# Kernel optimization log

Measured on AMD Instinct MI355X. Metric: run time of the kernel, lower is better.

Reference implementation:

```python
import jax, jax.numpy as jnp
import numpy as np

N = 50000
E = 800000
B = 64
NODE_IN, EDGE_IN, H, OUT_DIM = 16, 8, 64, 2


def _glorot(key, shape):
    fan_in, fan_out = shape[0], shape[-1]
    s = jnp.sqrt(6.0 / (fan_in + fan_out))
    return jax.random.uniform(key, shape, jnp.float32, -s, s)


def setup_inputs() -> dict:
    key = jax.random.key(0)
    ks = jax.random.split(key, 32)
    inp = {
        'x': jax.random.normal(ks[0], (N, NODE_IN), jnp.float32),
        'edge_index': jax.random.randint(ks[1], (2, E), 0, N).astype(jnp.int64),
        'edge_attr': jax.random.normal(ks[2], (E, EDGE_IN), jnp.float32),
        'batch': jnp.sort(jax.random.randint(ks[3], (N,), 0, B)).astype(jnp.int64),
        # encoders
        'W_node': _glorot(ks[4], (NODE_IN, H)), 'b_node': jnp.zeros((H,), jnp.float32),
        'W_edge': _glorot(ks[5], (EDGE_IN, H)), 'b_edge': jnp.zeros((H,), jnp.float32),
        # conv1: GATv2, heads=4, concat=True, edge_dim=H
        'Wl1': _glorot(ks[6], (H, 4 * H)), 'bl1': jnp.zeros((4 * H,), jnp.float32),
        'Wr1': _glorot(ks[7], (H, 4 * H)), 'br1': jnp.zeros((4 * H,), jnp.float32),
        'We1': _glorot(ks[8], (H, 4 * H)),
        'att1': _glorot(ks[9], (4, H)),
        'bias1': jnp.zeros((4 * H,), jnp.float32),
        # conv2: GATv2, heads=1, concat=False, in=4H
        'Wl2': _glorot(ks[10], (4 * H, H)), 'bl2': jnp.zeros((H,), jnp.float32),
        'Wr2': _glorot(ks[11], (4 * H, H)), 'br2': jnp.zeros((H,), jnp.float32),
        'We2': _glorot(ks[12], (H, H)),
        'att2': _glorot(ks[13], (1, H)),
        'bias2': jnp.zeros((H,), jnp.float32),
        # decoder
        'Wd1': _glorot(ks[14], (H, H)), 'bd1': jnp.zeros((H,), jnp.float32),
        'Wd2': _glorot(ks[15], (H, OUT_DIM)), 'bd2': jnp.zeros((OUT_DIM,), jnp.float32),
    }
    return inp


def _gatv2(x, src, dst, eattr, Wl, bl, Wr, br, We, att, bias, heads, out_ch, concat):
    n = x.shape[0]
    # add self-loops with edge_attr fill_value='mean' (segment mean over dst), PyG default
    ones = jnp.ones((src.shape[0],), x.dtype)
    deg = jax.ops.segment_sum(ones, dst, num_segments=n)
    loop_attr = jax.ops.segment_sum(eattr, dst, num_segments=n) / jnp.clip(deg, 1.0)[:, None]
    ea = jnp.concatenate([eattr, loop_attr], 0)               # [E+N, F_e]
    s = jnp.concatenate([src, jnp.arange(n)], 0)
    d = jnp.concatenate([dst, jnp.arange(n)], 0)
    xl = (x @ Wl + bl).reshape(n, heads, out_ch)              # source transform
    xr = (x @ Wr + br).reshape(n, heads, out_ch)              # target transform
    ep = (ea @ We).reshape(-1, heads, out_ch)                 # edge transform (no bias)
    m = jax.nn.leaky_relu(xl[s] + xr[d] + ep, 0.2)            # [E+N, heads, out_ch]
    logits = jnp.einsum('ehc,hc->eh', m, att)
    lmax = jax.ops.segment_max(logits, d, num_segments=n)
    lmax = jnp.where(jnp.isfinite(lmax), lmax, 0.0)
    a = jnp.exp(logits - lmax[d])
    denom = jax.ops.segment_sum(a, d, num_segments=n)
    alpha = a / (denom[d] + 1e-16)                            # segment softmax over dst
    out = jax.ops.segment_sum(alpha[..., None] * xl[s], d, num_segments=n)
    out = out.reshape(n, heads * out_ch) if concat else out.mean(1)
    return out + bias


def reference(x, edge_index, edge_attr, batch, W_node, b_node, W_edge, b_edge,
              Wl1, bl1, Wr1, br1, We1, att1, bias1,
              Wl2, bl2, Wr2, br2, We2, att2, bias2,
              Wd1, bd1, Wd2, bd2):
    src, dst = edge_index[0], edge_index[1]
    h = x @ W_node + b_node
    ea = edge_attr @ W_edge + b_edge
    h = jax.nn.elu(_gatv2(h, src, dst, ea, Wl1, bl1, Wr1, br1, We1, att1, bias1, 4, H, True))
    h = _gatv2(h, src, dst, ea, Wl2, bl2, Wr2, br2, We2, att2, bias2, 1, H, False)
    # global mean pool over batch vector
    cnt = jax.ops.segment_sum(jnp.ones((h.shape[0],), h.dtype), batch, num_segments=B)
    pooled = jax.ops.segment_sum(h, batch, num_segments=B) / jnp.clip(cnt, 1.0)[:, None]
    out = jax.nn.relu(pooled @ Wd1 + bd1) @ Wd2 + bd2
    return jax.nn.sigmoid(out)
```

## Files before the change

### kernel.cpp

```cpp
#include <hip/hip_runtime.h>
#include <math.h>

#define NN 50000
#define NE 800000
#define NB 64

__device__ __forceinline__ int permpos(int c) {
  return ((c & 63) << 2) | (((c >> 6) ^ c) & 3);
}

__device__ __forceinline__ unsigned short f2bf(float f) {
  unsigned int u = __float_as_uint(f);
  u += 0x7fffu + ((u >> 16) & 1u);
  return (unsigned short)(u >> 16);
}
__device__ __forceinline__ float bf2f(unsigned short b) {
  return __uint_as_float(((unsigned int)b) << 16);
}

__global__ void k_zero(int* __restrict__ p, int n) {
  int i = blockIdx.x * blockDim.x + threadIdx.x;
  if (i < n) p[i] = 0;
}

__global__ void k_fuse(const float* __restrict__ Wn, const float* __restrict__ bn,
                       const float* __restrict__ We, const float* __restrict__ be,
                       const float* __restrict__ Wl1, const float* __restrict__ bl1,
                       const float* __restrict__ Wr1, const float* __restrict__ br1,
                       const float* __restrict__ We1, const float* __restrict__ We2,
                       const float* __restrict__ att1, const float* __restrict__ bias1,
                       float* __restrict__ wl1e, float* __restrict__ bl1e,
                       float* __restrict__ wr1e, float* __restrict__ br1e,
                       float* __restrict__ wfe1, float* __restrict__ bfe1,
                       float* __restrict__ wfe2, float* __restrict__ bfe2,
                       float* __restrict__ att1p, float* __restrict__ bias1p) {
  int t = blockIdx.x * blockDim.x + threadIdx.x;
  if (t < 4096) {
    int i = t >> 8, j = t & 255; float s = 0.f;
    for (int k = 0; k < 64; k++) s += Wn[i * 64 + k] * Wl1[k * 256 + j];
    wl1e[i * 256 + permpos(j)] = s;
  } else if (t < 8192) {
    int u = t - 4096; int i = u >> 8, j = u & 255; float s = 0.f;
    for (int k = 0; k < 64; k++) s += Wn[i * 64 + k] * Wr1[k * 256 + j];
    wr1e[i * 256 + permpos(j)] = s;
  } else if (t < 10240) {
    int u = t - 8192; int i = u >> 8, j = u & 255; float s = 0.f;
    for (int k = 0; k < 64; k++) s += We[i * 64 + k] * We1[k * 256 + j];
    wfe1[i * 256 + permpos(j)] = s;
  } else if (t < 10752) {
    int u = t - 10240; int i = u >> 6, j = u & 63; float s = 0.f;
    for (int k = 0; k < 64; k++) s += We[i * 64 + k] * We2[k * 64 + j];
    wfe2[u] = s;
  } else if (t < 11008) {
    int j = t - 10752; float s = bl1[j];
    for (int k = 0; k < 64; k++) s += bn[k] * Wl1[k * 256 + j];
    bl1e[permpos(j)] = s;
  } else if (t < 11264) {
    int j = t - 11008; float s = br1[j];
    for (int k = 0; k < 64; k++) s += bn[k] * Wr1[k * 256 + j];
    br1e[permpos(j)] = s;
  } else if (t < 11520) {
    int j = t - 11264; float s = 0.f;
    for (int k = 0; k < 64; k++) s += be[k] * We1[k * 256 + j];
    bfe1[permpos(j)] = s;
  } else if (t < 11584) {
    int j = t - 11520; float s = 0.f;
    for (int k = 0; k < 64; k++) s += be[k] * We2[k * 64 + j];
    bfe2[j] = s;
  } else if (t < 11840) {
    int j = t - 11584;
    att1p[permpos(j)] = att1[j];
  } else if (t < 12096) {
    int j = t - 11840;
    bias1p[permpos(j)] = bias1[j];
  }
}

__global__ void k_deg(const int* __restrict__ dstA, int* __restrict__ deg) {
  int e = blockIdx.x * blockDim.x + threadIdx.x;
  if (e < NE) atomicAdd(&deg[dstA[e]], 1);
}

__global__ __launch_bounds__(1024) void k_scan1(const int* __restrict__ deg,
                                                int* __restrict__ incl, int* __restrict__ partials) {
  __shared__ int sm[1024];
  int i = blockIdx.x * 1024 + threadIdx.x;
  int v = (i < NN) ? (deg[i] + 1) : 0;
  sm[threadIdx.x] = v;
  __syncthreads();
  for (int off = 1; off < 1024; off <<= 1) {
    int t = (threadIdx.x >= off) ? sm[threadIdx.x - off] : 0;
    __syncthreads();
    sm[threadIdx.x] += t;
    __syncthreads();
  }
  if (i < NN) incl[i] = sm[threadIdx.x];
  if (threadIdx.x == 1023) partials[blockIdx.x] = sm[1023];
}

__global__ void k_scan2(int* __restrict__ partials, int* __restrict__ rowptr, int nblk) {
  int t = threadIdx.x;
  int v = (t < nblk) ? partials[t] : 0;
  for (int off = 1; off < 64; off <<= 1) {
    int u = __shfl_up(v, off, 64);
    if (t >= off) v += u;
  }
  if (t < nblk) partials[t] = v;
  if (t == nblk - 1) rowptr[NN] = v;
}

__global__ void k_scan3(const int* __restrict__ deg, const int* __restrict__ incl,
                        const int* __restrict__ partials, int* __restrict__ rowptr) {
  int i = blockIdx.x * blockDim.x + threadIdx.x;
  if (i >= NN) return;
  int blk = i >> 10;
  int base = blk ? partials[blk - 1] : 0;
  rowptr[i] = base + incl[i] - (deg[i] + 1);
}

__global__ void k_csr(const int* __restrict__ srcA, const int* __restrict__ dstA,
                      const int* __restrict__ rowptr, const int* __restrict__ deg,
                      int* __restrict__ cursor, int2* __restrict__ csr) {
  int t = blockIdx.x * blockDim.x + threadIdx.x;
  if (t < NE) {
    int d = dstA[t];
    int pos = rowptr[d] + atomicAdd(&cursor[d], 1);
    csr[pos] = make_int2(t, srcA[t]);
  } else if (t < NE + NN) {
    int n = t - NE;
    csr[rowptr[n] + deg[n]] = make_int2(NE + n, n);
  }
}

__global__ __launch_bounds__(256) void k_loop8(const int* __restrict__ rowptr,
                                               const int2* __restrict__ csr,
                                               const float* __restrict__ eattr,
                                               float* __restrict__ lattr) {
  int d = (blockIdx.x * blockDim.x + threadIdx.x) >> 6;
  int lane = threadIdx.x & 63;
  if (d >= NN) return;
  int beg = rowptr[d], endReal = rowptr[d + 1] - 1;
  int k = lane & 7, sub = lane >> 3;
  float s = 0.f;
  for (int i = beg + sub; i < endReal; i += 8) {
    int eid = csr[i].x;
    s += eattr[(size_t)eid * 8 + k];
  }
  s += __shfl_xor(s, 8, 64);
  s += __shfl_xor(s, 16, 64);
  s += __shfl_xor(s, 32, 64);
  float invdeg = 1.f / fmaxf((float)(endReal - beg), 1.f);
  if (lane < 8) lattr[(size_t)d * 8 + lane] = s * invdeg;
}

__global__ __launch_bounds__(256) void k_lin1(const float* __restrict__ x,
                                              const float* __restrict__ wl, const float* __restrict__ bl,
                                              const float* __restrict__ wr, const float* __restrict__ br,
                                              unsigned short* __restrict__ xl, float* __restrict__ xr) {
  __shared__ float xs[4][16];
  int nb = blockIdx.x * 4;
  int t = threadIdx.x;
  if (t < 64) xs[t >> 4][t & 15] = x[nb * 16 + t];
  __syncthreads();
  int w = t >> 6, lane = t & 63, l4 = lane << 2;
  float4 accl = *(const float4*)(bl + l4);
  float4 accr = *(const float4*)(br + l4);
  const float* xrow = xs[w];
#pragma unroll
  for (int k = 0; k < 16; k++) {
    float xv = xrow[k];
    float4 wl4 = *(const float4*)(wl + k * 256 + l4);
    float4 wr4 = *(const float4*)(wr + k * 256 + l4);
    accl.x += xv * wl4.x; accl.y += xv * wl4.y; accl.z += xv * wl4.z; accl.w += xv * wl4.w;
    accr.x += xv * wr4.x; accr.y += xv * wr4.y; accr.z += xv * wr4.z; accr.w += xv * wr4.w;
  }
  int node = nb + w;
  ushort4 us;
  us.x = f2bf(accl.x); us.y = f2bf(accl.y); us.z = f2bf(accl.z); us.w = f2bf(accl.w);
  *(ushort4*)(xl + (size_t)node * 256 + l4) = us;
  *(float4*)(xr + (size_t)node * 256 + l4) = accr;
}

__device__ __forceinline__ const float* ek_ptr(const float* __restrict__ eattr,
                                               const float* __restrict__ lattr, int eid) {
  return (eid < NE) ? (eattr + (size_t)eid * 8) : (lattr + (size_t)(eid - NE) * 8);
}

__device__ __forceinline__ float jreduce(float part[4]) {
  part[0] += __shfl_xor(part[1], 1, 64);
  part[2] += __shfl_xor(part[3], 1, 64);
  float v = part[0] + __shfl_xor(part[2], 2, 64);
  v += __shfl_xor(v, 4, 64);
  v += __shfl_xor(v, 8, 64);
  v += __shfl_xor(v, 16, 64);
  v += __shfl_xor(v, 32, 64);
  return v;
}

__global__ __launch_bounds__(256) void k_conv1(
    const float* __restrict__ eattr, const float* __restrict__ lattr,
    const int* __restrict__ rowptr, const int2* __restrict__ csr,
    const unsigned short* __restrict__ xl, const float* __restrict__ xrg,
    const float* __restrict__ att1p, const float* __restrict__ bias1p,
    const float* __restrict__ wfe1, const float* __restrict__ bfe1,
    float* __restrict__ out1) {
  int d = __builtin_amdgcn_readfirstlane((blockIdx.x * blockDim.x + threadIdx.x) >> 6);
  int lane = threadIdx.x & 63;
  if (d >= NN) return;
  int l4 = lane << 2;
  float4 xr4 = *(const float4*)(xrg + (size_t)d * 256 + l4);
  float4 at4 = *(const float4*)(att1p + l4);
  float4 bf4 = *(const float4*)(bfe1 + l4);
  float4 wf[8];
#pragma unroll
  for (int k = 0; k < 8; k++) wf[k] = *(const float4*)(wfe1 + k * 256 + l4);

  float acc0 = 0.f, acc1 = 0.f, acc2 = 0.f, acc3 = 0.f;
  float mrun = -INFINITY, lrun = 0.f;
  int beg = rowptr[d], end = rowptr[d + 1];

  auto ld4 = [&](int s) -> float4 {
    ushort4 u = *(const ushort4*)(xl + (size_t)s * 256 + l4);
    float4 f; f.x = bf2f(u.x); f.y = bf2f(u.y); f.z = bf2f(u.z); f.w = bf2f(u.w);
    return f;
  };
  auto epart = [&](const float* __restrict__ p, const float4& x4, float part[4]) {
    float e0 = bf4.x, e1 = bf4.y, e2 = bf4.z, e3 = bf4.w;
#pragma unroll
    for (int k = 0; k < 8; k++) {
      float ekv = p[k];
      e0 += ekv * wf[k].x; e1 += ekv * wf[k].y;
      e2 += ekv * wf[k].z; e3 += ekv * wf[k].w;
    }
    float m0 = x4.x + xr4.x + e0; m0 = (m0 > 0.f) ? m0 : 0.2f * m0;
    float m1 = x4.y + xr4.y + e1; m1 = (m1 > 0.f) ? m1 : 0.2f * m1;
    float m2 = x4.z + xr4.z + e2; m2 = (m2 > 0.f) ? m2 : 0.2f * m2;
    float m3 = x4.w + xr4.w + e3; m3 = (m3 > 0.f) ? m3 : 0.2f * m3;
    part[0] = at4.x * m0; part[1] = at4.y * m1;
    part[2] = at4.z * m2; part[3] = at4.w * m3;
  };

  int idx = beg;
  for (; idx + 4 <= end; idx += 4) {
    int2 e0 = csr[idx], e1 = csr[idx + 1], e2 = csr[idx + 2], e3 = csr[idx + 3];
    int s0 = __builtin_amdgcn_readfirstlane(e0.y), id0 = __builtin_amdgcn_readfirstlane(e0.x);
    int s1 = __builtin_amdgcn_readfirstlane(e1.y), id1 = __builtin_amdgcn_readfirstlane(e1.x);
    int s2 = __builtin_amdgcn_readfirstlane(e2.y), id2 = __builtin_amdgcn_readfirstlane(e2.x);
    int s3 = __builtin_amdgcn_readfirstlane(e3.y), id3 = __builtin_amdgcn_readfirstlane(e3.x);
    float4 x0 = ld4(s0), x1 = ld4(s1), x2 = ld4(s2), x3 = ld4(s3);
    float pa[4], pb[4], pc[4], pd[4];
    epart(ek_ptr(eattr, lattr, id0), x0, pa);
    epart(ek_ptr(eattr, lattr, id1), x1, pb);
    epart(ek_ptr(eattr, lattr, id2), x2, pc);
    epart(ek_ptr(eattr, lattr, id3), x3, pd);
    float v0 = jreduce(pa), v1 = jreduce(pb), v2 = jreduce(pc), v3 = jreduce(pd);
    float gmax = fmaxf(fmaxf(v0, v1), fmaxf(v2, v3));
    if (__ballot(gmax > mrun)) {
      float nm = fmaxf(mrun, gmax);
      float sc = __expf(mrun - nm);
      mrun = nm; lrun *= sc;
      float sc1 = __shfl_xor(sc, 1, 64);
      float sc2 = __shfl_xor(sc, 2, 64);
      float sc3 = __shfl_xor(sc1, 2, 64);
      acc0 *= sc; acc1 *= sc1; acc2 *= sc2; acc3 *= sc3;
    }
    float q0 = __expf(v0 - mrun), q1 = __expf(v1 - mrun);
    float q2 = __expf(v2 - mrun), q3 = __expf(v3 - mrun);
    lrun += q0 + q1 + q2 + q3;
    {
      float a1 = __shfl_xor(q0, 1, 64), a2 = __shfl_xor(q0, 2, 64), a3 = __shfl_xor(a1, 2, 64);
      acc0 += q0 * x0.x; acc1 += a1 * x0.y; acc2 += a2 * x0.z; acc3 += a3 * x0.w;
    }
    {
      float a1 = __shfl_xor(q1, 1, 64), a2 = __shfl_xor(q1, 2, 64), a3 = __shfl_xor(a1, 2, 64);
      acc0 += q1 * x1.x; acc1 += a1 * x1.y; acc2 += a2 * x1.z; acc3 += a3 * x1.w;
    }
    {
      float a1 = __shfl_xor(q2, 1, 64), a2 = __shfl_xor(q2, 2, 64), a3 = __shfl_xor(a1, 2, 64);
      acc0 += q2 * x2.x; acc1 += a1 * x2.y; acc2 += a2 * x2.z; acc3 += a3 * x2.w;
    }
    {
      float a1 = __shfl_xor(q3, 1, 64), a2 = __shfl_xor(q3, 2, 64), a3 = __shfl_xor(a1, 2, 64);
      acc0 += q3 * x3.x; acc1 += a1 * x3.y; acc2 += a2 * x3.z; acc3 += a3 * x3.w;
    }
  }
  for (; idx < end; ++idx) {
    int2 e0 = csr[idx];
    int s0 = __builtin_amdgcn_readfirstlane(e0.y), id0 = __builtin_amdgcn_readfirstlane(e0.x);
    float4 x0 = ld4(s0);
    float pa[4];
    epart(ek_ptr(eattr, lattr, id0), x0, pa);
    float v0 = jreduce(pa);
    if (__ballot(v0 > mrun)) {
      float nm = fmaxf(mrun, v0);
      float sc = __expf(mrun - nm);
      mrun = nm; lrun *= sc;
      float sc1 = __shfl_xor(sc, 1, 64);
      float sc2 = __shfl_xor(sc, 2, 64);
      float sc3 = __shfl_xor(sc1, 2, 64);
      acc0 *= sc; acc1 *= sc1; acc2 *= sc2; acc3 *= sc3;
    }
    float q0 = __expf(v0 - mrun);
    lrun += q0;
    float a1 = __shfl_xor(q0, 1, 64), a2 = __shfl_xor(q0, 2, 64), a3 = __shfl_xor(a1, 2, 64);
    acc0 += q0 * x0.x; acc1 += a1 * x0.y; acc2 += a2 * x0.z; acc3 += a3 * x0.w;
  }

  float lr0 = lrun;
  float lr1 = __shfl_xor(lr0, 1, 64);
  float lr2 = __shfl_xor(lr0, 2, 64);
  float lr3 = __shfl_xor(lr1, 2, 64);
  float4 bi4 = *(const float4*)(bias1p + l4);
  float4 o;
  o.x = acc0 / (lr0 + 1e-16f) + bi4.x;
  o.y = acc1 / (lr1 + 1e-16f) + bi4.y;
  o.z = acc2 / (lr2 + 1e-16f) + bi4.z;
  o.w = acc3 / (lr3 + 1e-16f) + bi4.w;
  o.x = (o.x > 0.f) ? o.x : (__expf(o.x) - 1.f);
  o.y = (o.y > 0.f) ? o.y : (__expf(o.y) - 1.f);
  o.z = (o.z > 0.f) ? o.z : (__expf(o.z) - 1.f);
  o.w = (o.w > 0.f) ? o.w : (__expf(o.w) - 1.f);
  *(float4*)(out1 + (size_t)d * 256 + l4) = o;
}

__global__ __launch_bounds__(256) void k_lin2(const float* __restrict__ in,
                                              const float* __restrict__ wl, const float* __restrict__ bl,
                                              const float* __restrict__ wr, const float* __restrict__ br,
                                              unsigned short* __restrict__ xl, float* __restrict__ xr) {
  int col = threadIdx.x & 63;
  int grp = threadIdx.x >> 6;
  int node0 = blockIdx.x * 32 + grp * 8;
  float sl[8], sr[8];
  float blv = bl[col], brv = br[col];
#pragma unroll
  for (int u = 0; u < 8; u++) { sl[u] = blv; sr[u] = brv; }
  const float4* r[8];
#pragma unroll
  for (int u = 0; u < 8; u++) r[u] = (const float4*)(in + (size_t)(node0 + u) * 256);
#pragma unroll 2
  for (int g4 = 0; g4 < 64; g4++) {
    int b = g4 & 3;
    int i0 = ((0 ^ b) << 6) + g4;
    int i1 = ((1 ^ b) << 6) + g4;
    int i2 = ((2 ^ b) << 6) + g4;
    int i3 = ((3 ^ b) << 6) + g4;
    float wl0 = wl[i0 * 64 + col], wl1v = wl[i1 * 64 + col];
    float wl2v = wl[i2 * 64 + col], wl3v = wl[i3 * 64 + col];
    float wr0 = wr[i0 * 64 + col], wr1v = wr[i1 * 64 + col];
    float wr2v = wr[i2 * 64 + col], wr3v = wr[i3 * 64 + col];
#pragma unroll
    for (int u = 0; u < 8; u++) {
      float4 v = r[u][g4];
      sl[u] += v.x * wl0 + v.y * wl1v + v.z * wl2v + v.w * wl3v;
      sr[u] += v.x * wr0 + v.y * wr1v + v.z * wr2v + v.w * wr3v;
    }
  }
#pragma unroll
  for (int u = 0; u < 8; u++) {
    int node = node0 + u;
    if (node < NN) {
      xl[(size_t)node * 64 + col] = f2bf(sl[u]);
      xr[(size_t)node * 64 + col] = sr[u];
    }
  }
}

__global__ __launch_bounds__(256) void k_conv2(
    const float* __restrict__ eattr, const float* __restrict__ lattr,
    const int* __restrict__ rowptr, const int2* __restrict__ csr,
    const unsigned short* __restrict__ xl, const float* __restrict__ xrg,
    const float* __restrict__ att2, const float* __restrict__ bias2,
    const float* __restrict__ wfe2, const float* __restrict__ bfe2,
    float* __restrict__ out2) {
  int d = __builtin_amdgcn_readfirstlane((blockIdx.x * blockDim.x + threadIdx.x) >> 6);
  int lane = threadIdx.x & 63;
  if (d >= NN) return;
  float xr_l = xrg[(size_t)d * 64 + lane];
  float att_l = att2[lane];
  float bfe_l = bfe2[lane];
  float wfe_l[8];
#pragma unroll
  for (int k = 0; k < 8; k++) wfe_l[k] = wfe2[k * 64 + lane];
  float acc = 0.f, mrun = -INFINITY, lrun = 0.f;
  int beg = rowptr[d], end = rowptr[d + 1];
  bool b0 = (lane & 1), b1 = (lane & 2);

  auto pl = [&](const float* __restrict__ p, float xs) {
    float ep = bfe_l;
#pragma unroll
    for (int k = 0; k < 8; k++) ep += p[k] * wfe_l[k];
    float m = xs + xr_l + ep;
    m = (m > 0.f) ? m : 0.2f * m;
    return att_l * m;
  };

  int idx = beg;
  for (; idx + 4 <= end; idx += 4) {
    int2 e0 = csr[idx], e1 = csr[idx + 1], e2 = csr[idx + 2], e3 = csr[idx + 3];
    int s0 = __builtin_amdgcn_readfirstlane(e0.y), id0 = __builtin_amdgcn_readfirstlane(e0.x);
    int s1 = __builtin_amdgcn_readfirstlane(e1.y), id1 = __builtin_amdgcn_readfirstlane(e1.x);
    int s2 = __builtin_amdgcn_readfirstlane(e2.y), id2 = __builtin_amdgcn_readfirstlane(e2.x);
    int s3 = __builtin_amdgcn_readfirstlane(e3.y), id3 = __builtin_amdgcn_readfirstlane(e3.x);
    float x0 = bf2f(xl[(size_t)s0 * 64 + lane]);
    float x1 = bf2f(xl[(size_t)s1 * 64 + lane]);
    float x2 = bf2f(xl[(size_t)s2 * 64 + lane]);
    float x3 = bf2f(xl[(size_t)s3 * 64 + lane]);
    float v0 = pl(ek_ptr(eattr, lattr, id0), x0);
    float v1 = pl(ek_ptr(eattr, lattr, id1), x1);
    float v2 = pl(ek_ptr(eattr, lattr, id2), x2);
    float v3 = pl(ek_ptr(eattr, lattr, id3), x3);
    float a01 = b0 ? v1 : v0;
    a01 += __shfl_xor(b0 ? v0 : v1, 1, 64);
    float a23 = b0 ? v3 : v2;
    a23 += __shfl_xor(b0 ? v2 : v3, 1, 64);
    float w = b1 ? a23 : a01;
    w += __shfl_xor(b1 ? a01 : a23, 2, 64);
    w += __shfl_xor(w, 4, 64);
    w += __shfl_xor(w, 8, 64);
    w += __shfl_xor(w, 16, 64);
    w += __shfl_xor(w, 32, 64);
    float g = fmaxf(w, __shfl_xor(w, 1, 64));
    g = fmaxf(g, __shfl_xor(g, 2, 64));
    if (g > mrun) {
      float sc = __expf(mrun - g);
      mrun = g; lrun *= sc; acc *= sc;
    }
    float q = __expf(w - mrun);
    float q1 = __shfl_xor(q, 1, 64);
    float q2 = __shfl_xor(q, 2, 64);
    float q3 = __shfl_xor(q1, 2, 64);
    lrun += (q + q1) + (q2 + q3);
    float u01 = b0 ? x1 : x0, u10 = b0 ? x0 : x1;
    float u23 = b0 ? x3 : x2, u32 = b0 ? x2 : x3;
    float xr0 = b1 ? u23 : u01;
    float xr1v = b1 ? u32 : u10;
    float xr2v = b1 ? u01 : u23;
    float xr3v = b1 ? u10 : u32;
    acc += q * xr0 + q1 * xr1v + q2 * xr2v + q3 * xr3v;
  }
  for (; idx < end; ++idx) {
    int2 e0 = csr[idx];
    int s0 = __builtin_amdgcn_readfirstlane(e0.y), id0 = __builtin_amdgcn_readfirstlane(e0.x);
    float x0 = bf2f(xl[(size_t)s0 * 64 + lane]);
    float v = pl(ek_ptr(eattr, lattr, id0), x0);
    v += __shfl_xor(v, 1, 64);
    v += __shfl_xor(v, 2, 64);
    v += __shfl_xor(v, 4, 64);
    v += __shfl_xor(v, 8, 64);
    v += __shfl_xor(v, 16, 64);
    v += __shfl_xor(v, 32, 64);
    if (v > mrun) {
      float sc = __expf(mrun - v);
      mrun = v; lrun *= sc; acc *= sc;
    }
    float q = __expf(v - mrun);
    lrun += q;
    acc += q * x0;
  }
  out2[(size_t)d * 64 + lane] = acc / (lrun + 1e-16f) + bias2[lane];
}

__device__ __forceinline__ int lowerb(const int* a, int n, int v) {
  int lo = 0, hi = n;
  while (lo < hi) {
    int mid = (lo + hi) >> 1;
    if (a[mid] < v) lo = mid + 1; else hi = mid;
  }
  return lo;
}

__global__ __launch_bounds__(256) void k_pool(const int* __restrict__ batch,
                                              const float* __restrict__ out2,
                                              float* __restrict__ pooled) {
  int b = blockIdx.x;
  int start = lowerb(batch, NN, b);
  int end = lowerb(batch, NN, b + 1);
  int c = threadIdx.x & 63, sub = threadIdx.x >> 6;
  float s = 0.f;
  for (int i = start + sub; i < end; i += 4) s += out2[(size_t)i * 64 + c];
  __shared__ float sm[256];
  sm[threadIdx.x] = s;
  __syncthreads();
  if (sub == 0) {
    float tot = sm[c] + sm[64 + c] + sm[128 + c] + sm[192 + c];
    float cnt = fmaxf((float)(end - start), 1.f);
    pooled[b * 64 + c] = tot / cnt;
  }
}

__global__ __launch_bounds__(1024) void k_dec(const float* __restrict__ pooled,
                                              const float* __restrict__ Wd1, const float* __restrict__ bd1,
                                              const float* __restrict__ Wd2, const float* __restrict__ bd2,
                                              float* __restrict__ out) {
  __shared__ float hid[64 * 64];
  int t = threadIdx.x;
  for (int i = t; i < 4096; i += 1024) {
    int b = i >> 6, j = i & 63;
    float s = bd1[j];
#pragma unroll 8
    for (int k = 0; k < 64; k++) s += pooled[b * 64 + k] * Wd1[k * 64 + j];
    hid[i] = fmaxf(s, 0.f);
  }
  __syncthreads();
  if (t < 128) {
    int b = t >> 1, o = t & 1;
    float s = bd2[o];
#pragma unroll 8
    for (int k = 0; k < 64; k++) s += hid[b * 64 + k] * Wd2[k * 2 + o];
    out[t] = 1.f / (1.f + __expf(-s));
  }
}

extern "C" void kernel_launch(void* const* d_in, const int* in_sizes, int n_in,
                              void* d_out, int out_size, void* d_ws, size_t ws_size,
                              hipStream_t stream) {
  const float* x     = (const float*)d_in[0];
  const int*   eidx  = (const int*)d_in[1];
  const float* eattr = (const float*)d_in[2];
  const int*   batch = (const int*)d_in[3];
  const float* Wn    = (const float*)d_in[4];
  const float* bn    = (const float*)d_in[5];
  const float* We    = (const float*)d_in[6];
  const float* be    = (const float*)d_in[7];
  const float* Wl1   = (const float*)d_in[8];
  const float* bl1   = (const float*)d_in[9];
  const float* Wr1   = (const float*)d_in[10];
  const float* br1   = (const float*)d_in[11];
  const float* We1   = (const float*)d_in[12];
  const float* att1  = (const float*)d_in[13];
  const float* bias1 = (const float*)d_in[14];
  const float* Wl2   = (const float*)d_in[15];
  const float* bl2   = (const float*)d_in[16];
  const float* Wr2   = (const float*)d_in[17];
  const float* br2   = (const float*)d_in[18];
  const float* We2   = (const float*)d_in[19];
  const float* att2  = (const float*)d_in[20];
  const float* bias2 = (const float*)d_in[21];
  const float* Wd1   = (const float*)d_in[22];
  const float* bd1   = (const float*)d_in[23];
  const float* Wd2   = (const float*)d_in[24];
  const float* bd2   = (const float*)d_in[25];

  const int* srcA = eidx;
  const int* dstA = eidx + NE;

  char* ws = (char*)d_ws;
  size_t off = 0;
  auto alloc = [&](size_t bytes) -> char* {
    char* p = ws + off;
    off += (bytes + 255) & ~(size_t)255;
    return p;
  };

  int*   deg    = (int*)alloc(NN * 4);
  int*   cursor = (int*)alloc(NN * 4);
  size_t zero_bytes = off;
  int*   rowptr   = (int*)alloc((NN + 1) * 4);
  int*   incl     = (int*)alloc(NN * 4);
  int*   partials = (int*)alloc(64 * 4);
  int2*  csr      = (int2*)alloc((size_t)(NE + NN + 1) * 8);
  float* lattr = (float*)alloc((size_t)NN * 8 * 4);
  float* wl1e  = (float*)alloc(4096 * 4);
  float* wr1e  = (float*)alloc(4096 * 4);
  float* wfe1  = (float*)alloc(2048 * 4);
  float* wfe2  = (float*)alloc(512 * 4);
  float* bl1e  = (float*)alloc(256 * 4);
  float* br1e  = (float*)alloc(256 * 4);
  float* bfe1  = (float*)alloc(256 * 4);
  float* bfe2  = (float*)alloc(64 * 4);
  float* att1p = (float*)alloc(256 * 4);
  float* bias1p= (float*)alloc(256 * 4);
  unsigned short* xl1 = (unsigned short*)alloc((size_t)NN * 256 * 2);
  float* xr1   = (float*)alloc((size_t)NN * 256 * 4);
  float* out1  = (float*)alloc((size_t)NN * 256 * 4);
  unsigned short* xl2 = (unsigned short*)alloc((size_t)NN * 64 * 2);
  float* xr2   = (float*)alloc((size_t)NN * 64 * 4);
  float* out2  = (float*)alloc((size_t)NN * 64 * 4);
  float* pooled = (float*)alloc((size_t)NB * 64 * 4);

  int zn = (int)(zero_bytes / 4);
  int nscan = (NN + 1023) / 1024;
  k_zero<<<(zn + 255) / 256, 256, 0, stream>>>((int*)d_ws, zn);
  k_fuse<<<(12096 + 255) / 256, 256, 0, stream>>>(Wn, bn, We, be, Wl1, bl1, Wr1, br1, We1, We2,
                                                  att1, bias1,
                                                  wl1e, bl1e, wr1e, br1e, wfe1, bfe1, wfe2, bfe2,
                                                  att1p, bias1p);
  k_deg<<<(NE + 255) / 256, 256, 0, stream>>>(dstA, deg);
  k_scan1<<<nscan, 1024, 0, stream>>>(deg, incl, partials);
  k_scan2<<<1, 64, 0, stream>>>(partials, rowptr, nscan);
  k_scan3<<<(NN + 255) / 256, 256, 0, stream>>>(deg, incl, partials, rowptr);
  k_csr<<<(NE + NN + 255) / 256, 256, 0, stream>>>(srcA, dstA, rowptr, deg, cursor, csr);
  k_loop8<<<(NN + 3) / 4, 256, 0, stream>>>(rowptr, csr, eattr, lattr);
  k_lin1<<<NN / 4, 256, 0, stream>>>(x, wl1e, bl1e, wr1e, br1e, xl1, xr1);
  k_conv1<<<(NN + 3) / 4, 256, 0, stream>>>(eattr, lattr, rowptr, csr, xl1, xr1,
                                            att1p, bias1p, wfe1, bfe1, out1);
  k_lin2<<<(NN + 31) / 32, 256, 0, stream>>>(out1, Wl2, bl2, Wr2, br2, xl2, xr2);
  k_conv2<<<(NN + 3) / 4, 256, 0, stream>>>(eattr, lattr, rowptr, csr, xl2, xr2,
                                            att2, bias2, wfe2, bfe2, out2);
  k_pool<<<NB, 256, 0, stream>>>(batch, out2, pooled);
  k_dec<<<1, 1024, 0, stream>>>(pooled, Wd1, bd1, Wd2, bd2, (float*)d_out);
}
```

Baseline: 771.7 us.

## Use fp16 edge features with fdot2, fold edge bias into xr, use exp2

Edge attributes and self-loop mean attributes are converted to packed fp16 and the fused edge weights are stored as half2 pairs, so the per-edge projections in both conv kernels run on fdot2 and read half the edge bytes. The constant edge-bias terms are folded into the right-projection biases (br1e and k_lin2's xr bias), which removes the per-edge bias add. Attention vectors are pre-scaled by log2(e) so the softmax uses exp2f. This adds an extra conversion pass over the 800k edges and lowers the edge-projection precision to fp16.

```diff
diff --git a/kernel.cpp b/kernel.cpp
--- a/kernel.cpp
+++ b/kernel.cpp
@@ -4,9 +4,25 @@
 #define NN 50000
 #define NE 800000
 #define NB 64
+#define LOG2E 1.4426950408889634f
+
+typedef _Float16 h2 __attribute__((ext_vector_type(2)));
+
+#if __has_builtin(__builtin_amdgcn_fdot2)
+__device__ __forceinline__ float FDOT2(h2 a, h2 b, float c) {
+  return __builtin_amdgcn_fdot2(a, b, c, false);
+}
+#else
+__device__ __forceinline__ float FDOT2(h2 a, h2 b, float c) {
+  return c + (float)a.x * (float)b.x + (float)a.y * (float)b.y;
+}
+#endif
 
 __device__ __forceinline__ int permpos(int c) {
   return ((c & 63) << 2) | (((c >> 6) ^ c) & 3);
+}
+__device__ __forceinline__ int invpos(int p) {
+  return ((((p & 3) ^ ((p >> 2) & 3)) & 3) << 6) | (p >> 2);
 }
 
 __device__ __forceinline__ unsigned short f2bf(float f) {
@@ -29,11 +45,13 @@
                        const float* __restrict__ Wr1, const float* __restrict__ br1,
                        const float* __restrict__ We1, const float* __restrict__ We2,
                        const float* __restrict__ att1, const float* __restrict__ bias1,
+                       const float* __restrict__ att2,
                        float* __restrict__ wl1e, float* __restrict__ bl1e,
                        float* __restrict__ wr1e, float* __restrict__ br1e,
-                       float* __restrict__ wfe1, float* __restrict__ bfe1,
-                       float* __restrict__ wfe2, float* __restrict__ bfe2,
-                       float* __restrict__ att1p, float* __restrict__ bias1p) {
+                       h2* __restrict__ wfh1, h2* __restrict__ wfh2,
+                       float* __restrict__ bfe2,
+                       float* __restrict__ att1p, float* __restrict__ att2p,
+                       float* __restrict__ bias1p) {
   int t = blockIdx.x * blockDim.x + threadIdx.x;
   if (t < 4096) {
     int i = t >> 8, j = t & 255; float s = 0.f;
@@ -43,37 +61,63 @@
     int u = t - 4096; int i = u >> 8, j = u & 255; float s = 0.f;
     for (int k = 0; k < 64; k++) s += Wn[i * 64 + k] * Wr1[k * 256 + j];
     wr1e[i * 256 + permpos(j)] = s;
-  } else if (t < 10240) {
-    int u = t - 8192; int i = u >> 8, j = u & 255; float s = 0.f;
-    for (int k = 0; k < 64; k++) s += We[i * 64 + k] * We1[k * 256 + j];
-    wfe1[i * 256 + permpos(j)] = s;
-  } else if (t < 10752) {
-    int u = t - 10240; int i = u >> 6, j = u & 63; float s = 0.f;
-    for (int k = 0; k < 64; k++) s += We[i * 64 + k] * We2[k * 64 + j];
-    wfe2[u] = s;
-  } else if (t < 11008) {
-    int j = t - 10752; float s = bl1[j];
+  } else if (t < 9216) {
+    int u = t - 8192;
+    int k2 = u >> 8, p = u & 255;
+    int c = invpos(p);
+    float lo = 0.f, hi = 0.f;
+    for (int k = 0; k < 64; k++) {
+      lo += We[(2 * k2) * 64 + k] * We1[k * 256 + c];
+      hi += We[(2 * k2 + 1) * 64 + k] * We1[k * 256 + c];
+    }
+    h2 v; v.x = (_Float16)lo; v.y = (_Float16)hi;
+    wfh1[u] = v;
+  } else if (t < 9472) {
+    int u = t - 9216;
+    int k2 = u >> 6, c = u & 63;
+    float lo = 0.f, hi = 0.f;
+    for (int k = 0; k < 64; k++) {
+      lo += We[(2 * k2) * 64 + k] * We2[k * 64 + c];
+      hi += We[(2 * k2 + 1) * 64 + k] * We2[k * 64 + c];
+    }
+    h2 v; v.x = (_Float16)lo; v.y = (_Float16)hi;
+    wfh2[u] = v;
+  } else if (t < 9728) {
+    int j = t - 9472; float s = bl1[j];
     for (int k = 0; k < 64; k++) s += bn[k] * Wl1[k * 256 + j];
     bl1e[permpos(j)] = s;
-  } else if (t < 11264) {
-    int j = t - 11008; float s = br1[j];
+  } else if (t < 9984) {
+    int j = t - 9728; float s = br1[j];
     for (int k = 0; k < 64; k++) s += bn[k] * Wr1[k * 256 + j];
+    for (int k = 0; k < 64; k++) s += be[k] * We1[k * 256 + j];
     br1e[permpos(j)] = s;
-  } else if (t < 11520) {
-    int j = t - 11264; float s = 0.f;
-    for (int k = 0; k < 64; k++) s += be[k] * We1[k * 256 + j];
-    bfe1[permpos(j)] = s;
-  } else if (t < 11584) {
-    int j = t - 11520; float s = 0.f;
+  } else if (t < 10048) {
+    int j = t - 9984; float s = 0.f;
     for (int k = 0; k < 64; k++) s += be[k] * We2[k * 64 + j];
     bfe2[j] = s;
-  } else if (t < 11840) {
-    int j = t - 11584;
-    att1p[permpos(j)] = att1[j];
-  } else if (t < 12096) {
-    int j = t - 11840;
+  } else if (t < 10304) {
+    int j = t - 10048;
+    att1p[permpos(j)] = att1[j] * LOG2E;
+  } else if (t < 10368) {
+    int j = t - 10304;
+    att2p[j] = att2[j] * LOG2E;
+  } else if (t < 10624) {
+    int j = t - 10368;
     bias1p[permpos(j)] = bias1[j];
   }
+}
+
+__global__ void k_toh(const float* __restrict__ eattr, h2* __restrict__ ehalf) {
+  int e = blockIdx.x * blockDim.x + threadIdx.x;
+  if (e >= NE) return;
+  float4 a = *(const float4*)(eattr + (size_t)e * 8);
+  float4 b = *(const float4*)(eattr + (size_t)e * 8 + 4);
+  h2 o[4];
+  o[0].x = (_Float16)a.x; o[0].y = (_Float16)a.y;
+  o[1].x = (_Float16)a.z; o[1].y = (_Float16)a.w;
+  o[2].x = (_Float16)b.x; o[2].y = (_Float16)b.y;
+  o[3].x = (_Float16)b.z; o[3].y = (_Float16)b.w;
+  *(uint4*)(ehalf + (size_t)e * 4) = *(uint4*)o;
 }
 
 __global__ void k_deg(const int* __restrict__ dstA, int* __restrict__ deg) {
@@ -135,7 +179,7 @@
 __global__ __launch_bounds__(256) void k_loop8(const int* __restrict__ rowptr,
                                                const int2* __restrict__ csr,
                                                const float* __restrict__ eattr,
-                                               float* __restrict__ lattr) {
+                                               h2* __restrict__ lattrh) {
   int d = (blockIdx.x * blockDim.x + threadIdx.x) >> 6;
   int lane = threadIdx.x & 63;
   if (d >= NN) return;
@@ -150,7 +194,12 @@
   s += __shfl_xor(s, 16, 64);
   s += __shfl_xor(s, 32, 64);
   float invdeg = 1.f / fmaxf((float)(endReal - beg), 1.f);
-  if (lane < 8) lattr[(size_t)d * 8 + lane] = s * invdeg;
+  s *= invdeg;
+  float nxt = __shfl_down(s, 1, 64);
+  if (lane < 8 && !(lane & 1)) {
+    h2 v; v.x = (_Float16)s; v.y = (_Float16)nxt;
+    lattrh[(size_t)d * 4 + (lane >> 1)] = v;
+  }
 }
 
 __global__ __launch_bounds__(256) void k_lin1(const float* __restrict__ x,
@@ -181,9 +230,9 @@
   *(float4*)(xr + (size_t)node * 256 + l4) = accr;
 }
 
-__device__ __forceinline__ const float* ek_ptr(const float* __restrict__ eattr,
-                                               const float* __restrict__ lattr, int eid) {
-  return (eid < NE) ? (eattr + (size_t)eid * 8) : (lattr + (size_t)(eid - NE) * 8);
+__device__ __forceinline__ const h2* ekh_ptr(const h2* __restrict__ ehalf,
+                                             const h2* __restrict__ lattrh, int eid) {
+  return (eid < NE) ? (ehalf + (size_t)eid * 4) : (lattrh + (size_t)(eid - NE) * 4);
 }
 
 __device__ __forceinline__ float jreduce(float part[4]) {
@@ -198,11 +247,11 @@
 }
 
 __global__ __launch_bounds__(256) void k_conv1(
-    const float* __restrict__ eattr, const float* __restrict__ lattr,
+    const h2* __restrict__ ehalf, const h2* __restrict__ lattrh,
     const int* __restrict__ rowptr, const int2* __restrict__ csr,
     const unsigned short* __restrict__ xl, const float* __restrict__ xrg,
     const float* __restrict__ att1p, const float* __restrict__ bias1p,
-    const float* __restrict__ wfe1, const float* __restrict__ bfe1,
+    const h2* __restrict__ wfh1,
     float* __restrict__ out1) {
   int d = __builtin_amdgcn_readfirstlane((blockIdx.x * blockDim.x + threadIdx.x) >> 6);
   int lane = threadIdx.x & 63;
@@ -210,10 +259,12 @@
   int l4 = lane << 2;
   float4 xr4 = *(const float4*)(xrg + (size_t)d * 256 + l4);
   float4 at4 = *(const float4*)(att1p + l4);
-  float4 bf4 = *(const float4*)(bfe1 + l4);
-  float4 wf[8];
-#pragma unroll
-  for (int k = 0; k < 8; k++) wf[k] = *(const float4*)(wfe1 + k * 256 + l4);
+  h2 wf[4][4];
+#pragma unroll
+  for (int k2 = 0; k2 < 4; k2++) {
+#pragma unroll
+    for (int slot = 0; slot < 4; slot++) wf[slot][k2] = wfh1[k2 * 256 + l4 + slot];
+  }
 
   float acc0 = 0.f, acc1 = 0.f, acc2 = 0.f, acc3 = 0.f;
   float mrun = -INFINITY, lrun = 0.f;
@@ -224,14 +275,17 @@
     float4 f; f.x = bf2f(u.x); f.y = bf2f(u.y); f.z = bf2f(u.z); f.w = bf2f(u.w);
     return f;
   };
-  auto epart = [&](const float* __restrict__ p, const float4& x4, float part[4]) {
-    float e0 = bf4.x, e1 = bf4.y, e2 = bf4.z, e3 = bf4.w;
-#pragma unroll
-    for (int k = 0; k < 8; k++) {
-      float ekv = p[k];
-      e0 += ekv * wf[k].x; e1 += ekv * wf[k].y;
-      e2 += ekv * wf[k].z; e3 += ekv * wf[k].w;
-    }
+  auto epart = [&](const h2* __restrict__ p, const float4& x4, float part[4]) {
+    h2 a0 = p[0], a1 = p[1], a2 = p[2], a3 = p[3];
+    float e0 = 0.f, e1 = 0.f, e2 = 0.f, e3 = 0.f;
+    e0 = FDOT2(wf[0][0], a0, e0); e0 = FDOT2(wf[0][1], a1, e0);
+    e0 = FDOT2(wf[0][2], a2, e0); e0 = FDOT2(wf[0][3], a3, e0);
+    e1 = FDOT2(wf[1][0], a0, e1); e1 = FDOT2(wf[1][1], a1, e1);
+    e1 = FDOT2(wf[1][2], a2, e1); e1 = FDOT2(wf[1][3], a3, e1);
+    e2 = FDOT2(wf[2][0], a0, e2); e2 = FDOT2(wf[2][1], a1, e2);
+    e2 = FDOT2(wf[2][2], a2, e2); e2 = FDOT2(wf[2][3], a3, e2);
+    e3 = FDOT2(wf[3][0], a0, e3); e3 = FDOT2(wf[3][1], a1, e3);
+    e3 = FDOT2(wf[3][2], a2, e3); e3 = FDOT2(wf[3][3], a3, e3);
     float m0 = x4.x + xr4.x + e0; m0 = (m0 > 0.f) ? m0 : 0.2f * m0;
     float m1 = x4.y + xr4.y + e1; m1 = (m1 > 0.f) ? m1 : 0.2f * m1;
     float m2 = x4.z + xr4.z + e2; m2 = (m2 > 0.f) ? m2 : 0.2f * m2;
@@ -249,24 +303,24 @@
     int s3 = __builtin_amdgcn_readfirstlane(e3.y), id3 = __builtin_amdgcn_readfirstlane(e3.x);
     float4 x0 = ld4(s0), x1 = ld4(s1), x2 = ld4(s2), x3 = ld4(s3);
     float pa[4], pb[4], pc[4], pd[4];
-    epart(ek_ptr(eattr, lattr, id0), x0, pa);
-    epart(ek_ptr(eattr, lattr, id1), x1, pb);
-    epart(ek_ptr(eattr, lattr, id2), x2, pc);
-    epart(ek_ptr(eattr, lattr, id3), x3, pd);
+    epart(ekh_ptr(ehalf, lattrh, id0), x0, pa);
+    epart(ekh_ptr(ehalf, lattrh, id1), x1, pb);
+    epart(ekh_ptr(ehalf, lattrh, id2), x2, pc);
+    epart(ekh_ptr(ehalf, lattrh, id3), x3, pd);
     float v0 = jreduce(pa), v1 = jreduce(pb), v2 = jreduce(pc), v3 = jreduce(pd);
     float gmax = fmaxf(fmaxf(v0, v1), fmaxf(v2, v3));
     if (__ballot(gmax > mrun)) {
       float nm = fmaxf(mrun, gmax);
-      float sc = __expf(mrun - nm);
+      float sc = exp2f(mrun - nm);
       mrun = nm; lrun *= sc;
       float sc1 = __shfl_xor(sc, 1, 64);
       float sc2 = __shfl_xor(sc, 2, 64);
       float sc3 = __shfl_xor(sc1, 2, 64);
       acc0 *= sc; acc1 *= sc1; acc2 *= sc2; acc3 *= sc3;
     }
-    float q0 = __expf(v0 - mrun), q1 = __expf(v1 - mrun);
-    float q2 = __expf(v2 - mrun), q3 = __expf(v3 - mrun);
-    lrun += q0 + q1 + q2 + q3;
+    float q0 = exp2f(v0 - mrun), q1 = exp2f(v1 - mrun);
+    float q2 = exp2f(v2 - mrun), q3 = exp2f(v3 - mrun);
+    lrun += (q0 + q1) + (q2 + q3);
     {
       float a1 = __shfl_xor(q0, 1, 64), a2 = __shfl_xor(q0, 2, 64), a3 = __shfl_xor(a1, 2, 64);
       acc0 += q0 * x0.x; acc1 += a1 * x0.y; acc2 += a2 * x0.z; acc3 += a3 * x0.w;
@@ -289,18 +343,18 @@
     int s0 = __builtin_amdgcn_readfirstlane(e0.y), id0 = __builtin_amdgcn_readfirstlane(e0.x);
     float4 x0 = ld4(s0);
     float pa[4];
-    epart(ek_ptr(eattr, lattr, id0), x0, pa);
+    epart(ekh_ptr(ehalf, lattrh, id0), x0, pa);
     float v0 = jreduce(pa);
     if (__ballot(v0 > mrun)) {
       float nm = fmaxf(mrun, v0);
-      float sc = __expf(mrun - nm);
+      float sc = exp2f(mrun - nm);
       mrun = nm; lrun *= sc;
       float sc1 = __shfl_xor(sc, 1, 64);
       float sc2 = __shfl_xor(sc, 2, 64);
       float sc3 = __shfl_xor(sc1, 2, 64);
       acc0 *= sc; acc1 *= sc1; acc2 *= sc2; acc3 *= sc3;
     }
-    float q0 = __expf(v0 - mrun);
+    float q0 = exp2f(v0 - mrun);
     lrun += q0;
     float a1 = __shfl_xor(q0, 1, 64), a2 = __shfl_xor(q0, 2, 64), a3 = __shfl_xor(a1, 2, 64);
     acc0 += q0 * x0.x; acc1 += a1 * x0.y; acc2 += a2 * x0.z; acc3 += a3 * x0.w;
@@ -326,12 +380,13 @@
 __global__ __launch_bounds__(256) void k_lin2(const float* __restrict__ in,
                                               const float* __restrict__ wl, const float* __restrict__ bl,
                                               const float* __restrict__ wr, const float* __restrict__ br,
+                                              const float* __restrict__ bfe2,
                                               unsigned short* __restrict__ xl, float* __restrict__ xr) {
   int col = threadIdx.x & 63;
   int grp = threadIdx.x >> 6;
   int node0 = blockIdx.x * 32 + grp * 8;
   float sl[8], sr[8];
-  float blv = bl[col], brv = br[col];
+  float blv = bl[col], brv = br[col] + bfe2[col];
 #pragma unroll
   for (int u = 0; u < 8; u++) { sl[u] = blv; sr[u] = brv; }
   const float4* r[8];
@@ -366,29 +421,29 @@
 }
 
 __global__ __launch_bounds__(256) void k_conv2(
-    const float* __restrict__ eattr, const float* __restrict__ lattr,
+    const h2* __restrict__ ehalf, const h2* __restrict__ lattrh,
     const int* __restrict__ rowptr, const int2* __restrict__ csr,
     const unsigned short* __restrict__ xl, const float* __restrict__ xrg,
-    const float* __restrict__ att2, const float* __restrict__ bias2,
-    const float* __restrict__ wfe2, const float* __restrict__ bfe2,
+    const float* __restrict__ att2p, const float* __restrict__ bias2,
+    const h2* __restrict__ wfh2,
     float* __restrict__ out2) {
   int d = __builtin_amdgcn_readfirstlane((blockIdx.x * blockDim.x + threadIdx.x) >> 6);
   int lane = threadIdx.x & 63;
   if (d >= NN) return;
   float xr_l = xrg[(size_t)d * 64 + lane];
-  float att_l = att2[lane];
-  float bfe_l = bfe2[lane];
-  float wfe_l[8];
-#pragma unroll
-  for (int k = 0; k < 8; k++) wfe_l[k] = wfe2[k * 64 + lane];
+  float att_l = att2p[lane];
+  h2 wfh_l[4];
+#pragma unroll
+  for (int k2 = 0; k2 < 4; k2++) wfh_l[k2] = wfh2[k2 * 64 + lane];
   float acc = 0.f, mrun = -INFINITY, lrun = 0.f;
   int beg = rowptr[d], end = rowptr[d + 1];
   bool b0 = (lane & 1), b1 = (lane & 2);
 
-  auto pl = [&](const float* __restrict__ p, float xs) {
-    float ep = bfe_l;
-#pragma unroll
-    for (int k = 0; k < 8; k++) ep += p[k] * wfe_l[k];
+  auto pl = [&](const h2* __restrict__ p, float xs) {
+    h2 a0 = p[0], a1 = p[1], a2 = p[2], a3 = p[3];
+    float ep = 0.f;
+    ep = FDOT2(wfh_l[0], a0, ep); ep = FDOT2(wfh_l[1], a1, ep);
+    ep = FDOT2(wfh_l[2], a2, ep); ep = FDOT2(wfh_l[3], a3, ep);
     float m = xs + xr_l + ep;
     m = (m > 0.f) ? m : 0.2f * m;
     return att_l * m;
@@ -405,10 +460,10 @@
     float x1 = bf2f(xl[(size_t)s1 * 64 + lane]);
     float x2 = bf2f(xl[(size_t)s2 * 64 + lane]);
     float x3 = bf2f(xl[(size_t)s3 * 64 + lane]);
-    float v0 = pl(ek_ptr(eattr, lattr, id0), x0);
-    float v1 = pl(ek_ptr(eattr, lattr, id1), x1);
-    float v2 = pl(ek_ptr(eattr, lattr, id2), x2);
-    float v3 = pl(ek_ptr(eattr, lattr, id3), x3);
+    float v0 = pl(ekh_ptr(ehalf, lattrh, id0), x0);
+    float v1 = pl(ekh_ptr(ehalf, lattrh, id1), x1);
+    float v2 = pl(ekh_ptr(ehalf, lattrh, id2), x2);
+    float v3 = pl(ekh_ptr(ehalf, lattrh, id3), x3);
     float a01 = b0 ? v1 : v0;
     a01 += __shfl_xor(b0 ? v0 : v1, 1, 64);
     float a23 = b0 ? v3 : v2;
@@ -422,10 +477,10 @@
     float g = fmaxf(w, __shfl_xor(w, 1, 64));
     g = fmaxf(g, __shfl_xor(g, 2, 64));
     if (g > mrun) {
-      float sc = __expf(mrun - g);
+      float sc = exp2f(mrun - g);
       mrun = g; lrun *= sc; acc *= sc;
     }
-    float q = __expf(w - mrun);
+    float q = exp2f(w - mrun);
     float q1 = __shfl_xor(q, 1, 64);
     float q2 = __shfl_xor(q, 2, 64);
     float q3 = __shfl_xor(q1, 2, 64);
@@ -442,7 +497,7 @@
     int2 e0 = csr[idx];
     int s0 = __builtin_amdgcn_readfirstlane(e0.y), id0 = __builtin_amdgcn_readfirstlane(e0.x);
     float x0 = bf2f(xl[(size_t)s0 * 64 + lane]);
-    float v = pl(ek_ptr(eattr, lattr, id0), x0);
+    float v = pl(ekh_ptr(ehalf, lattrh, id0), x0);
     v += __shfl_xor(v, 1, 64);
     v += __shfl_xor(v, 2, 64);
     v += __shfl_xor(v, 4, 64);
@@ -450,10 +505,10 @@
     v += __shfl_xor(v, 16, 64);
     v += __shfl_xor(v, 32, 64);
     if (v > mrun) {
-      float sc = __expf(mrun - v);
+      float sc = exp2f(mrun - v);
       mrun = v; lrun *= sc; acc *= sc;
     }
-    float q = __expf(v - mrun);
+    float q = exp2f(v - mrun);
     lrun += q;
     acc += q * x0;
   }
@@ -559,44 +614,46 @@
   int*   incl     = (int*)alloc(NN * 4);
   int*   partials = (int*)alloc(64 * 4);
   int2*  csr      = (int2*)alloc((size_t)(NE + NN + 1) * 8);
-  float* lattr = (float*)alloc((size_t)NN * 8 * 4);
+  h2*    ehalf  = (h2*)alloc((size_t)NE * 4 * 4);
+  h2*    lattrh = (h2*)alloc((size_t)NN * 4 * 4);
   float* wl1e  = (float*)alloc(4096 * 4);
   float* wr1e  = (float*)alloc(4096 * 4);
-  float* wfe1  = (float*)alloc(2048 * 4);
-  float* wfe2  = (float*)alloc(512 * 4);
+  h2*    wfh1  = (h2*)alloc(1024 * 4);
+  h2*    wfh2  = (h2*)alloc(256 * 4);
   float* bl1e  = (float*)alloc(256 * 4);
   float* br1e  = (float*)alloc(256 * 4);
-  float* bfe1  = (float*)alloc(256 * 4);
   float* bfe2  = (float*)alloc(64 * 4);
   float* att1p = (float*)alloc(256 * 4);
+  float* att2p = (float*)alloc(64 * 4);
   float* bias1p= (float*)alloc(256 * 4);
   unsigned short* xl1 = (unsigned short*)alloc((size_t)NN * 256 * 2);
-  float* xr1   = (float*)alloc((size_t)NN * 256 * 4);
+  float* xrb1  = (float*)alloc((size_t)NN * 256 * 4);
   float* out1  = (float*)alloc((size_t)NN * 256 * 4);
   unsigned short* xl2 = (unsigned short*)alloc((size_t)NN * 64 * 2);
-  float* xr2   = (float*)alloc((size_t)NN * 64 * 4);
+  float* xrb2  = (float*)alloc((size_t)NN * 64 * 4);
   float* out2  = (float*)alloc((size_t)NN * 64 * 4);
   float* pooled = (float*)alloc((size_t)NB * 64 * 4);
 
   int zn = (int)(zero_bytes / 4);
   int nscan = (NN + 1023) / 1024;
   k_zero<<<(zn + 255) / 256, 256, 0, stream>>>((int*)d_ws, zn);
-  k_fuse<<<(12096 + 255) / 256, 256, 0, stream>>>(Wn, bn, We, be, Wl1, bl1, Wr1, br1, We1, We2,
-                                                  att1, bias1,
-                                                  wl1e, bl1e, wr1e, br1e, wfe1, bfe1, wfe2, bfe2,
-                                                  att1p, bias1p);
+  k_fuse<<<(10624 + 255) / 256, 256, 0, stream>>>(Wn, bn, We, be, Wl1, bl1, Wr1, br1, We1, We2,
+                                                  att1, bias1, att2,
+                                                  wl1e, bl1e, wr1e, br1e, wfh1, wfh2, bfe2,
+                                                  att1p, att2p, bias1p);
+  k_toh<<<(NE + 255) / 256, 256, 0, stream>>>(eattr, ehalf);
   k_deg<<<(NE + 255) / 256, 256, 0, stream>>>(dstA, deg);
   k_scan1<<<nscan, 1024, 0, stream>>>(deg, incl, partials);
   k_scan2<<<1, 64, 0, stream>>>(partials, rowptr, nscan);
   k_scan3<<<(NN + 255) / 256, 256, 0, stream>>>(deg, incl, partials, rowptr);
   k_csr<<<(NE + NN + 255) / 256, 256, 0, stream>>>(srcA, dstA, rowptr, deg, cursor, csr);
-  k_loop8<<<(NN + 3) / 4, 256, 0, stream>>>(rowptr, csr, eattr, lattr);
-  k_lin1<<<NN / 4, 256, 0, stream>>>(x, wl1e, bl1e, wr1e, br1e, xl1, xr1);
-  k_conv1<<<(NN + 3) / 4, 256, 0, stream>>>(eattr, lattr, rowptr, csr, xl1, xr1,
-                                            att1p, bias1p, wfe1, bfe1, out1);
-  k_lin2<<<(NN + 31) / 32, 256, 0, stream>>>(out1, Wl2, bl2, Wr2, br2, xl2, xr2);
-  k_conv2<<<(NN + 3) / 4, 256, 0, stream>>>(eattr, lattr, rowptr, csr, xl2, xr2,
-                                            att2, bias2, wfe2, bfe2, out2);
+  k_loop8<<<(NN + 3) / 4, 256, 0, stream>>>(rowptr, csr, eattr, lattrh);
+  k_lin1<<<NN / 4, 256, 0, stream>>>(x, wl1e, bl1e, wr1e, br1e, xl1, xrb1);
+  k_conv1<<<(NN + 3) / 4, 256, 0, stream>>>(ehalf, lattrh, rowptr, csr, xl1, xrb1,
+                                            att1p, bias1p, wfh1, out1);
+  k_lin2<<<(NN + 31) / 32, 256, 0, stream>>>(out1, Wl2, bl2, Wr2, br2, bfe2, xl2, xrb2);
+  k_conv2<<<(NN + 3) / 4, 256, 0, stream>>>(ehalf, lattrh, rowptr, csr, xl2, xrb2,
+                                            att2p, bias2, wfh2, out2);
   k_pool<<<NB, 256, 0, stream>>>(batch, out2, pooled);
   k_dec<<<1, 1024, 0, stream>>>(pooled, Wd1, bd1, Wd2, bd2, (float*)d_out);
 }
```

Result: faster. 734.4 us (-4.8%).
